# Kernel tuning notes

Hardware: AMD Instinct MI355X
Metric: run time of the kernel (lower is better)

The kernel has to match this reference:

```python
import jax, jax.numpy as jnp
import numpy as np

Q_MAX = 127.0  # 2**(8-1) - 1
EPS = 1e-08


def quantize_activation(x):
    # per-tensor symmetric int8 quant with STE
    scale = jnp.maximum(jnp.max(jnp.abs(x)) / Q_MAX, EPS)
    x_scaled = x / scale
    rounded = jnp.clip(jnp.round(x_scaled), -Q_MAX, Q_MAX)
    # STE: forward = rounded, backward = identity w.r.t. x_scaled
    q = x_scaled + jax.lax.stop_gradient(rounded - x_scaled)
    return q, jax.lax.stop_gradient(scale)


def ternarize_weight(W):
    scale = jnp.mean(jnp.abs(W)) + EPS
    W_norm = W / scale
    rounded = jnp.clip(jnp.round(W_norm), -1.0, 1.0)
    # STE: forward = rounded, backward = identity w.r.t. W
    tW = W + jax.lax.stop_gradient(rounded - W)
    return tW, jax.lax.stop_gradient(scale)


def setup_inputs() -> dict:
    key = jax.random.key(0)
    kx, kw = jax.random.split(key)
    in_features, out_features = 4096, 11008
    x = jax.random.normal(kx, (4, 2048, in_features), dtype=jnp.float32)
    # kaiming_uniform_(a=sqrt(5)) -> U(-bound, bound), bound = sqrt(6/((1+a^2)*fan_in)) = 1/sqrt(fan_in)
    bound = 1.0 / np.sqrt(in_features)
    W = jax.random.uniform(kw, (out_features, in_features), dtype=jnp.float32,
                           minval=-bound, maxval=bound)
    return {"x": x, "W": W}


def reference(x, W):
    qx, act_scale = quantize_activation(x)
    tW, w_scale = ternarize_weight(W)
    # F.linear: x @ W.T ; [b, s, in] x [out, in] -> [b, s, out]
    out = jnp.einsum('bsi,oi->bso', qx, tW)
    return out * (w_scale * act_scale)
```

## Files before the change

### kernel.cpp

```cpp
#include <hip/hip_runtime.h>
#include <cstdint>

typedef int i32x4 __attribute__((ext_vector_type(4)));
typedef int i32x16 __attribute__((ext_vector_type(16)));

#define M_DIM 8192
#define N_DIM 11008
#define K_DIM 4096
#define NT    (K_DIM / 128)

#define WS_AMAX_OFF   0
#define WS_WSUM_OFF   4096
#define WS_SCALES_OFF 12288
#define WS_QX_OFF     16384
#define WS_TW_OFF     (16384 + 33554432)

__device__ __forceinline__ void gload_lds16(const void* g, void* l) {
  __builtin_amdgcn_global_load_lds(
      (const __attribute__((address_space(1))) unsigned int*)g,
      (__attribute__((address_space(3))) unsigned int*)l, 16, 0, 0);
}


__global__ void reduce_amax(const float* __restrict__ x, float* __restrict__ partial, int n4) {
  const float4* xv = (const float4*)x;
  float m = 0.f;
  for (long i = (long)blockIdx.x * blockDim.x + threadIdx.x; i < n4;
       i += (long)gridDim.x * blockDim.x) {
    float4 v = xv[i];
    m = fmaxf(m, fmaxf(fmaxf(fabsf(v.x), fabsf(v.y)), fmaxf(fabsf(v.z), fabsf(v.w))));
  }
  __shared__ float sm[256];
  sm[threadIdx.x] = m;
  __syncthreads();
  for (int s = 128; s > 0; s >>= 1) {
    if (threadIdx.x < s) sm[threadIdx.x] = fmaxf(sm[threadIdx.x], sm[threadIdx.x + s]);
    __syncthreads();
  }
  if (threadIdx.x == 0) partial[blockIdx.x] = sm[0];
}

__global__ void reduce_wsum(const float* __restrict__ w, double* __restrict__ partial, int n4) {
  const float4* wv = (const float4*)w;
  double acc = 0.0;
  for (long i = (long)blockIdx.x * blockDim.x + threadIdx.x; i < n4;
       i += (long)gridDim.x * blockDim.x) {
    float4 v = wv[i];
    acc += (double)fabsf(v.x) + (double)fabsf(v.y) + (double)fabsf(v.z) + (double)fabsf(v.w);
  }
  __shared__ double sd[256];
  sd[threadIdx.x] = acc;
  __syncthreads();
  for (int s = 128; s > 0; s >>= 1) {
    if (threadIdx.x < s) sd[threadIdx.x] += sd[threadIdx.x + s];
    __syncthreads();
  }
  if (threadIdx.x == 0) partial[blockIdx.x] = sd[0];
}

__global__ void finalize_scales(const float* __restrict__ amax_p,
                                const double* __restrict__ wsum_p,
                                float* __restrict__ scales) {
  __shared__ float sm[1024];
  __shared__ double sd[1024];
  const int t = threadIdx.x;
  sm[t] = amax_p[t];
  sd[t] = wsum_p[t];
  __syncthreads();
  for (int s = 512; s > 0; s >>= 1) {
    if (t < s) {
      sm[t] = fmaxf(sm[t], sm[t + s]);
      sd[t] += sd[t + s];
    }
    __syncthreads();
  }
  if (t == 0) {
    float act_scale = fmaxf(sm[0] / 127.0f, 1e-8f);
    float w_scale = (float)(sd[0] / (double)((long long)N_DIM * K_DIM)) + 1e-8f;
    scales[0] = act_scale;
    scales[1] = w_scale;
    scales[2] = act_scale * w_scale;
  }
}


__device__ __forceinline__ int quant_clip(float v, float s, float lim) {
  float r = rintf(v / s);
  r = fminf(fmaxf(r, -lim), lim);
  return (int)r;
}

__global__ void quant_x(const float* __restrict__ x, const float* __restrict__ scales,
                        int8_t* __restrict__ q) {
  const float s = scales[0];
  const long i = (long)blockIdx.x * blockDim.x + threadIdx.x;
  const float4* xv = (const float4*)x + (i << 2);
  i32x4 pk;
#pragma unroll
  for (int j = 0; j < 4; ++j) {
    float4 v = xv[j];
    int b0 = quant_clip(v.x, s, 127.f);
    int b1 = quant_clip(v.y, s, 127.f);
    int b2 = quant_clip(v.z, s, 127.f);
    int b3 = quant_clip(v.w, s, 127.f);
    pk[j] = (b0 & 255) | ((b1 & 255) << 8) | ((b2 & 255) << 16) | (b3 << 24);
  }
  *((i32x4*)q + i) = pk;
}

__global__ void tern_w(const float* __restrict__ w, const float* __restrict__ scales,
                       int8_t* __restrict__ q) {
  const float s = scales[1];
  const long i = (long)blockIdx.x * blockDim.x + threadIdx.x;
  const float4* wv = (const float4*)w + (i << 2);
  i32x4 pk;
#pragma unroll
  for (int j = 0; j < 4; ++j) {
    float4 v = wv[j];
    int b0 = quant_clip(v.x, s, 1.f);
    int b1 = quant_clip(v.y, s, 1.f);
    int b2 = quant_clip(v.z, s, 1.f);
    int b3 = quant_clip(v.w, s, 1.f);
    pk[j] = (b0 & 255) | ((b1 & 255) << 8) | ((b2 & 255) << 16) | (b3 << 24);
  }
  *((i32x4*)q + i) = pk;
}


__global__ __launch_bounds__(512, 2) void gemm_i8(const int8_t* __restrict__ qx,
                                                  const int8_t* __restrict__ tw,
                                                  const float* __restrict__ scales,
                                                  float* __restrict__ out) {
  __shared__ __align__(16) int8_t lds[4][32768];

  const int tid = threadIdx.x;
  const int l = tid & 63;
  const int w = tid >> 6;

  const int bid = blockIdx.x;
  const int xcd = bid & 7;
  const int local = bid >> 3;
  const int ni = local >> 2;
  const int mi = (xcd << 2) + (local & 3);
  const long row0 = (long)mi << 8;
  const long col0 = (long)ni << 8;

  const int srow = tid >> 3;
  const int sch = (tid & 7) ^ (srow & 7);
  const int8_t* pA = qx + (row0 + srow) * (long)K_DIM + (sch << 4);
  const int8_t* pB = tw + (col0 + srow) * (long)K_DIM + (sch << 4);
  const int ldst = w << 10;

  auto stage = [&](int8_t* dA, int8_t* dB, int kt) {
    const long cb = (long)kt << 7;
#pragma unroll
    for (int i = 0; i < 4; ++i)
      gload_lds16(pA + cb + ((long)i * 64) * K_DIM, dA + i * 8192 + ldst);
#pragma unroll
    for (int i = 0; i < 4; ++i)
      gload_lds16(pB + cb + ((long)i * 64) * K_DIM, dB + i * 8192 + ldst);
  };

  const int lane31 = l & 31;
  const int khalf = l >> 5;
  const int swz = l & 7;
  int cOff[4];
#pragma unroll
  for (int ks = 0; ks < 4; ++ks) cOff[ks] = ((((ks << 1) | khalf) ^ swz) << 4);
  const int aRow = ((w >> 2) * 128 + lane31) * 128;
  int bRow[2];
  bRow[0] = ((w & 3) * 64 + lane31) * 128;
  bRow[1] = bRow[0] + 32 * 128;

  i32x16 acc[4][2];
#pragma unroll
  for (int mf = 0; mf < 4; ++mf)
#pragma unroll
    for (int nf = 0; nf < 2; ++nf)
#pragma unroll
      for (int e = 0; e < 16; ++e) acc[mf][nf][e] = 0;

  int8_t* cA = lds[0];
  int8_t* cB = lds[2];
  int8_t* nA = lds[1];
  int8_t* nB = lds[3];

  stage(cA, cB, 0);

  for (int kt = 0; kt < NT; ++kt) {
    if (kt + 1 < NT) {
      stage(nA, nB, kt + 1);
      asm volatile("s_waitcnt vmcnt(8)" ::: "memory");
    } else {
      asm volatile("s_waitcnt vmcnt(0)" ::: "memory");
    }
    __builtin_amdgcn_s_barrier();
    asm volatile("" ::: "memory");

    i32x4 bf[2][4];
#pragma unroll
    for (int nf = 0; nf < 2; ++nf)
#pragma unroll
      for (int ks = 0; ks < 4; ++ks)
        bf[nf][ks] = *(const i32x4*)(cB + bRow[nf] + cOff[ks]);

#pragma unroll
    for (int mf = 0; mf < 4; ++mf) {
      i32x4 af[4];
#pragma unroll
      for (int ks = 0; ks < 4; ++ks)
        af[ks] = *(const i32x4*)(cA + aRow + mf * 4096 + cOff[ks]);
      __builtin_amdgcn_s_setprio(1);
#pragma unroll
      for (int ks = 0; ks < 4; ++ks) {
        acc[mf][0] = __builtin_amdgcn_mfma_i32_32x32x32_i8(af[ks], bf[0][ks], acc[mf][0], 0, 0, 0);
        acc[mf][1] = __builtin_amdgcn_mfma_i32_32x32x32_i8(af[ks], bf[1][ks], acc[mf][1], 0, 0, 0);
      }
      __builtin_amdgcn_s_setprio(0);
    }

    asm volatile("s_waitcnt lgkmcnt(0)" ::: "memory");
    __builtin_amdgcn_s_barrier();
    asm volatile("" ::: "memory");

    int8_t* t;
    t = cA; cA = nA; nA = t;
    t = cB; cB = nB; nB = t;
  }

  const float osc = scales[2];
  const int rbase = khalf << 2;
#pragma unroll
  for (int mf = 0; mf < 4; ++mf)
#pragma unroll
    for (int nf = 0; nf < 2; ++nf)
#pragma unroll
      for (int reg = 0; reg < 16; ++reg) {
        int rr = (w >> 2) * 128 + mf * 32 + rbase + (reg & 3) + ((reg >> 2) << 3);
        int cc = (w & 3) * 64 + nf * 32 + lane31;
        out[(row0 + rr) * (long)N_DIM + (col0 + cc)] = (float)acc[mf][nf][reg] * osc;
      }
}


extern "C" void kernel_launch(void* const* d_in, const int* in_sizes, int n_in,
                              void* d_out, int out_size, void* d_ws, size_t ws_size,
                              hipStream_t stream) {
  const float* x = (const float*)d_in[0];
  const float* W = (const float*)d_in[1];
  float* out = (float*)d_out;

  char* ws = (char*)d_ws;
  float*  amax_p = (float*)(ws + WS_AMAX_OFF);
  double* wsum_p = (double*)(ws + WS_WSUM_OFF);
  float*  scales = (float*)(ws + WS_SCALES_OFF);
  int8_t* qx = (int8_t*)(ws + WS_QX_OFF);
  int8_t* tw = (int8_t*)(ws + WS_TW_OFF);

  reduce_amax<<<1024, 256, 0, stream>>>(x, amax_p, (M_DIM * (long)K_DIM) / 4);
  reduce_wsum<<<1024, 256, 0, stream>>>(W, wsum_p, (N_DIM * (long)K_DIM) / 4);
  finalize_scales<<<1, 1024, 0, stream>>>(amax_p, wsum_p, scales);
  quant_x<<<(M_DIM * (long)K_DIM) / 16 / 256, 256, 0, stream>>>(x, scales, qx);
  tern_w<<<(N_DIM * (long)K_DIM) / 16 / 256, 256, 0, stream>>>(W, scales, tw);

  const int grid = (M_DIM / 256) * (N_DIM / 256);
  gemm_i8<<<grid, 512, 0, stream>>>(qx, tw, scales, out);
}
```

Measured before the change: 563.2 us.

## Interleave prefetch loads with MFMA k-steps in a ping-pong schedule

Restructures the int8 GEMM main loop so that global-to-LDS prefetch of the next K tile is split into four parts, each issued alongside one k-step of MFMA work. The loop order changes from mf-outer to ks-outer, so each step loads only one set of A and B fragments before its MFMAs. The first part of tile t+2 is issued into the freed buffer at the end of each iteration. This aims to spread memory traffic and cut register pressure, but adds two barriers per k-step, eight per tile, which may cost more than the overlap gains.

```diff
diff --git a/kernel.cpp b/kernel.cpp
--- a/kernel.cpp
+++ b/kernel.cpp
@@ -151,14 +151,10 @@
   const int8_t* pB = tw + (col0 + srow) * (long)K_DIM + (sch << 4);
   const int ldst = w << 10;
 
-  auto stage = [&](int8_t* dA, int8_t* dB, int kt) {
+  auto stage_part = [&](int8_t* dA, int8_t* dB, int kt, int part) {
     const long cb = (long)kt << 7;
-#pragma unroll
-    for (int i = 0; i < 4; ++i)
-      gload_lds16(pA + cb + ((long)i * 64) * K_DIM, dA + i * 8192 + ldst);
-#pragma unroll
-    for (int i = 0; i < 4; ++i)
-      gload_lds16(pB + cb + ((long)i * 64) * K_DIM, dB + i * 8192 + ldst);
+    gload_lds16(pA + cb + ((long)part * 64) * K_DIM, dA + part * 8192 + ldst);
+    gload_lds16(pB + cb + ((long)part * 64) * K_DIM, dB + part * 8192 + ldst);
   };
 
   const int lane31 = l & 31;
@@ -168,9 +164,8 @@
 #pragma unroll
   for (int ks = 0; ks < 4; ++ks) cOff[ks] = ((((ks << 1) | khalf) ^ swz) << 4);
   const int aRow = ((w >> 2) * 128 + lane31) * 128;
-  int bRow[2];
-  bRow[0] = ((w & 3) * 64 + lane31) * 128;
-  bRow[1] = bRow[0] + 32 * 128;
+  const int bRow0 = ((w & 3) * 64 + lane31) * 128;
+  const int bRow1 = bRow0 + 32 * 128;
 
   i32x16 acc[4][2];
 #pragma unroll
@@ -180,52 +175,51 @@
 #pragma unroll
       for (int e = 0; e < 16; ++e) acc[mf][nf][e] = 0;
 
-  int8_t* cA = lds[0];
-  int8_t* cB = lds[2];
-  int8_t* nA = lds[1];
-  int8_t* nB = lds[3];
-
-  stage(cA, cB, 0);
-
-  for (int kt = 0; kt < NT; ++kt) {
-    if (kt + 1 < NT) {
-      stage(nA, nB, kt + 1);
-      asm volatile("s_waitcnt vmcnt(8)" ::: "memory");
-    } else {
-      asm volatile("s_waitcnt vmcnt(0)" ::: "memory");
-    }
-    __builtin_amdgcn_s_barrier();
-    asm volatile("" ::: "memory");
-
-    i32x4 bf[2][4];
-#pragma unroll
-    for (int nf = 0; nf < 2; ++nf)
-#pragma unroll
-      for (int ks = 0; ks < 4; ++ks)
-        bf[nf][ks] = *(const i32x4*)(cB + bRow[nf] + cOff[ks]);
-
-#pragma unroll
-    for (int mf = 0; mf < 4; ++mf) {
-      i32x4 af[4];
-#pragma unroll
-      for (int ks = 0; ks < 4; ++ks)
-        af[ks] = *(const i32x4*)(cA + aRow + mf * 4096 + cOff[ks]);
+#pragma unroll
+  for (int p = 0; p < 4; ++p) stage_part(lds[0], lds[2], 0, p);
+  stage_part(lds[1], lds[3], 1, 0);
+  asm volatile("s_waitcnt vmcnt(2)" ::: "memory");
+  __builtin_amdgcn_s_barrier();
+
+  for (int t = 0; t < NT; ++t) {
+    int8_t* cA = lds[t & 1];
+    int8_t* cB = lds[2 + (t & 1)];
+    int8_t* nA = lds[(t & 1) ^ 1];
+    int8_t* nB = lds[2 + ((t & 1) ^ 1)];
+    const bool pf = (t + 1 < NT);
+
+#pragma unroll
+    for (int ks = 0; ks < 4; ++ks) {
+      i32x4 af[4], b0, b1;
+#pragma unroll
+      for (int mf = 0; mf < 4; ++mf)
+        af[mf] = *(const i32x4*)(cA + aRow + mf * 4096 + cOff[ks]);
+      b0 = *(const i32x4*)(cB + bRow0 + cOff[ks]);
+      b1 = *(const i32x4*)(cB + bRow1 + cOff[ks]);
+      if (ks < 3 && pf) stage_part(nA, nB, t + 1, ks + 1);
+      asm volatile("" ::: "memory");
+      __builtin_amdgcn_s_barrier();
+      asm volatile("s_waitcnt lgkmcnt(0)" ::: "memory");
       __builtin_amdgcn_s_setprio(1);
 #pragma unroll
-      for (int ks = 0; ks < 4; ++ks) {
-        acc[mf][0] = __builtin_amdgcn_mfma_i32_32x32x32_i8(af[ks], bf[0][ks], acc[mf][0], 0, 0, 0);
-        acc[mf][1] = __builtin_amdgcn_mfma_i32_32x32x32_i8(af[ks], bf[1][ks], acc[mf][1], 0, 0, 0);
+      for (int mf = 0; mf < 4; ++mf) {
+        acc[mf][0] = __builtin_amdgcn_mfma_i32_32x32x32_i8(af[mf], b0, acc[mf][0], 0, 0, 0);
+        acc[mf][1] = __builtin_amdgcn_mfma_i32_32x32x32_i8(af[mf], b1, acc[mf][1], 0, 0, 0);
       }
       __builtin_amdgcn_s_setprio(0);
+      asm volatile("" ::: "memory");
+      __builtin_amdgcn_s_barrier();
     }
 
-    asm volatile("s_waitcnt lgkmcnt(0)" ::: "memory");
-    __builtin_amdgcn_s_barrier();
-    asm volatile("" ::: "memory");
-
-    int8_t* t;
-    t = cA; cA = nA; nA = t;
-    t = cB; cB = nB; nB = t;
+    if (pf) {
+      if (t + 2 < NT) {
+        stage_part(cA, cB, t + 2, 0);
+        asm volatile("s_waitcnt vmcnt(2)" ::: "memory");
+      } else {
+        asm volatile("s_waitcnt vmcnt(0)" ::: "memory");
+      }
+      __builtin_amdgcn_s_barrier();
+    }
   }
 
   const float osc = scales[2];
```

After: 541.7 us. 1.04x faster.
